# Kernel tuning notes

Measured on AMD Instinct MI355X. Metric: run time of the kernel, lower is better.

## Reference

```python
import jax, jax.numpy as jnp
import numpy as np
from jax import lax


def setup_inputs() -> dict:
    key = jax.random.key(0)
    ks = jax.random.split(key, 16)
    B, H, W, C = 4, 48, 48, 512
    N = H * W
    std = 0.02  # trunc_normal std in the torch init

    def nrm(k, shape, s=std):
        return jax.random.normal(k, shape, dtype=jnp.float32) * s

    return {
        "x": jax.random.normal(ks[0], (B, N, C), jnp.float32),
        "context": jax.random.normal(ks[1], (B, N, C), jnp.float32),
        "mask1": jax.random.uniform(ks[2], (B, N), jnp.float32),
        "mask2": jax.random.uniform(ks[3], (B, N), jnp.float32),
        "q_w": nrm(ks[4], (C, C)), "q_b": jnp.zeros((C,), jnp.float32),
        "kv1_w": nrm(ks[5], (C, C)), "kv1_b": jnp.zeros((C,), jnp.float32),
        "kv2_w": nrm(ks[6], (C, C)), "kv2_b": jnp.zeros((C,), jnp.float32),
        "f1_w": nrm(ks[7], (1, 48)), "f1_b": jnp.zeros((1,), jnp.float32),
        "f2_w": nrm(ks[8], (1, 12)), "f2_b": jnp.zeros((1,), jnp.float32),
        "lepe_w": nrm(ks[9], (C, C)), "lepe_b": jnp.zeros((C,), jnp.float32),
        "lepe_conv_w": nrm(ks[10], (C, 1, 3, 3), float(np.sqrt(2.0 / 9.0))),
        "lepe_conv_b": jnp.zeros((C,), jnp.float32),
        "proj_w": nrm(ks[11], (C, C)), "proj_b": jnp.zeros((C,), jnp.float32),
        "H": H, "W": W,
    }


def _lin(t, w, b):
    # torch nn.Linear: y = t @ W^T + b, W:[out,in]
    return t @ w.T + b


def _pooled_seq(ctx, idx, f1_w, f1_b, f2_w, f2_b):
    # ctx:[B,HW,C], idx:[B,HW] mask-sorted indices. sr_ratio==4 => groups of 48/12/1.
    B, HW, Cc = ctx.shape
    t1, t2 = HW // 192, HW // 24  # token1=(HW//48)//4, token2=(HW//12)//2
    g = jnp.take_along_axis(ctx, idx[:, :, None], axis=1)  # [B,HW,C] gathered
    p1 = g[:, : HW // 4].transpose(0, 2, 1).reshape(B, Cc, t1, 48)
    p2 = g[:, HW // 4 : 3 * HW // 4].transpose(0, 2, 1).reshape(B, Cc, t2, 12)
    p3 = g[:, 3 * HW // 4 :].transpose(0, 2, 1)  # [B,C,HW//4]
    a1 = (p1 @ f1_w.T)[..., 0] + f1_b  # [B,C,t1]
    a2 = (p2 @ f2_w.T)[..., 0] + f2_b  # [B,C,t2]
    return jnp.concatenate([a1, a2, p3], axis=-1).transpose(0, 2, 1)  # [B,Lkv,C]


def reference(x, context, mask1, mask2, q_w, q_b, kv1_w, kv1_b, kv2_w, kv2_b,
              f1_w, f1_b, f2_w, f2_b, lepe_w, lepe_b, lepe_conv_w, lepe_conv_b,
              proj_w, proj_b, H, W):
    B, N, C = x.shape
    nh = 8
    hd = C // nh
    scale = hd ** -0.5

    # lepe: linear + depthwise 3x3 conv positional encoding
    le = _lin(x, lepe_w, lepe_b).transpose(0, 2, 1).reshape(B, C, H, W)
    le = lax.conv_general_dilated(le, lepe_conv_w, (1, 1), ((1, 1), (1, 1)),
                                  dimension_numbers=("NCHW", "OIHW", "NCHW"),
                                  feature_group_count=C)
    lepe = (le + lepe_conv_b[None, :, None, None]).reshape(B, C, N).transpose(0, 2, 1)

    # mask-sorted grouped pooling of context (two orderings: row-major and transposed)
    idx1 = jnp.argsort(mask1, axis=1)
    idx2 = jnp.argsort(mask2, axis=1)
    ctx_t = context.reshape(B, H, W, C).transpose(0, 2, 1, 3).reshape(B, N, C)
    seq1 = _pooled_seq(context, idx1, f1_w, f1_b, f2_w, f2_b)
    seq2 = _pooled_seq(ctx_t, idx2, f1_w, f1_b, f2_w, f2_b)

    q = _lin(x, q_w, q_b).reshape(B, N, nh, hd).transpose(0, 2, 1, 3)  # [B,h,N,hd]
    kv1 = _lin(seq1, kv1_w, kv1_b).reshape(B, -1, 2, nh // 2, hd).transpose(2, 0, 3, 1, 4)
    kv2 = _lin(seq2, kv2_w, kv2_b).reshape(B, -1, 2, nh // 2, hd).transpose(2, 0, 3, 1, 4)
    k = jnp.concatenate([kv1[0], kv2[0]], axis=1)  # [B,h,Lkv,hd]
    v = jnp.concatenate([kv1[1], kv2[1]], axis=1)

    attn = jax.nn.softmax(jnp.einsum("bhnd,bhld->bhnl", q, k) * scale, axis=-1)
    out = jnp.einsum("bhnl,bhld->bhnd", attn, v).transpose(0, 2, 1, 3).reshape(B, N, C)
    return _lin(out + lepe, proj_w, proj_b)
```

## Files before the change

kernel.cpp:

```cpp
#include <hip/hip_runtime.h>
#include <hip/hip_bf16.h>
#include <math.h>

#define B_    4
#define H_    48
#define W_    48
#define N_    2304
#define C_    512
#define NH_   8
#define HD_   64
#define LKV_  684
#define LKP_  704

typedef __attribute__((ext_vector_type(8))) short short8;
typedef __attribute__((ext_vector_type(8))) unsigned short ushort8;
typedef __attribute__((ext_vector_type(4))) float f32x4;

#define MFMA16(a, b, c) __builtin_amdgcn_mfma_f32_16x16x32_bf16(a, b, c, 0, 0, 0)

__device__ __forceinline__ unsigned short f2bf(float f) {
  __hip_bfloat16 h = __float2bfloat16(f);
  return *reinterpret_cast<unsigned short*>(&h);
}
__device__ __forceinline__ float bf2f(unsigned short u) {
  unsigned int x = ((unsigned int)u) << 16;
  return *reinterpret_cast<float*>(&x);
}
__device__ __forceinline__ void gld16(const unsigned short* g, unsigned short* l) {
  __builtin_amdgcn_global_load_lds(
      (const __attribute__((address_space(1))) void*)g,
      (__attribute__((address_space(3))) void*)l, 16, 0, 0);
}

__global__ __launch_bounds__(256) void pack_all(
    const float* __restrict__ lepe_w, const float* __restrict__ q_w,
    const float* __restrict__ kv1_w, const float* __restrict__ kv2_w,
    const float* __restrict__ proj_w, const float* __restrict__ x,
    unsigned short* __restrict__ wb, unsigned short* __restrict__ xb)
{
  int i = (blockIdx.x * 256 + threadIdx.x) * 4;
  const float* s; unsigned short* d; int rel;
  if      (i < 262144)  { s = lepe_w; d = wb;           rel = i; }
  else if (i < 524288)  { s = q_w;    d = wb + 262144;  rel = i - 262144; }
  else if (i < 786432)  { s = kv1_w;  d = wb + 524288;  rel = i - 524288; }
  else if (i < 1048576) { s = kv2_w;  d = wb + 786432;  rel = i - 786432; }
  else if (i < 1310720) { s = proj_w; d = wb + 1048576; rel = i - 1048576; }
  else                  { s = x;      d = xb;           rel = i - 1310720; }
  float4 v = *(const float4*)(s + rel);
  ushort4 o;
  o.x = f2bf(v.x); o.y = f2bf(v.y); o.z = f2bf(v.z); o.w = f2bf(v.w);
  *(ushort4*)(d + rel) = o;
}

struct GPair {
  const unsigned short *A0, *A1, *B0, *B1;
  const float *bias0, *bias1;
  void *out0, *out1;
  int bf0, bf1;
  float sc0, sc1;
};

__global__ __launch_bounds__(256) void gemm_bf16(GPair p, int K, int Nn)
{
  const unsigned short* A  = blockIdx.z ? p.A1 : p.A0;
  const unsigned short* Bw = blockIdx.z ? p.B1 : p.B0;
  const float* bias        = blockIdx.z ? p.bias1 : p.bias0;
  void* out                = blockIdx.z ? p.out1 : p.out0;
  const int out_bf16       = blockIdx.z ? p.bf1 : p.bf0;
  const float oscale       = blockIdx.z ? p.sc1 : p.sc0;

  __shared__ unsigned short Abuf[128 * 32];
  __shared__ unsigned short Bbuf[128 * 32];
  const int tid = threadIdx.x;
  const int l = tid & 63, w = tid >> 6;
  const int wm = w >> 1, wn = w & 1;
  const int lo16 = l & 15, hi = l >> 4;
  const int row0 = blockIdx.x * 128, col0 = blockIdx.y * 128;
  const int srow = tid >> 2, scol = (tid & 3) * 8;

  const unsigned short* Asrc = A + (size_t)(row0 + srow) * K + scol;
  const unsigned short* Bsrc = Bw + (size_t)(col0 + srow) * K + scol;

  f32x4 acc[4][4];
  #pragma unroll
  for (int m = 0; m < 4; ++m)
    #pragma unroll
    for (int n = 0; n < 4; ++n)
      #pragma unroll
      for (int r = 0; r < 4; ++r) acc[m][n][r] = 0.f;

  for (int k0 = 0; k0 < K; k0 += 32) {
    __syncthreads();
    gld16(Asrc + k0,                   &Abuf[tid * 8]);
    gld16(Asrc + (size_t)64 * K + k0,  &Abuf[2048 + tid * 8]);
    gld16(Bsrc + k0,                   &Bbuf[tid * 8]);
    gld16(Bsrc + (size_t)64 * K + k0,  &Bbuf[2048 + tid * 8]);
    __syncthreads();
    short8 af[4], bf[4];
    #pragma unroll
    for (int m = 0; m < 4; ++m)
      af[m] = *(const short8*)&Abuf[(wm * 64 + m * 16 + lo16) * 32 + hi * 8];
    #pragma unroll
    for (int n = 0; n < 4; ++n)
      bf[n] = *(const short8*)&Bbuf[(wn * 64 + n * 16 + lo16) * 32 + hi * 8];
    #pragma unroll
    for (int m = 0; m < 4; ++m)
      #pragma unroll
      for (int n = 0; n < 4; ++n)
        acc[m][n] = MFMA16(af[m], bf[n], acc[m][n]);
  }

  #pragma unroll
  for (int m = 0; m < 4; ++m) {
    #pragma unroll
    for (int n = 0; n < 4; ++n) {
      int gcol = col0 + wn * 64 + n * 16 + lo16;
      #pragma unroll
      for (int r = 0; r < 4; ++r) {
        int grow = row0 + wm * 64 + m * 16 + hi * 4 + r;
        float v = acc[m][n][r] + bias[gcol];
        if (out_bf16)
          ((unsigned short*)out)[(size_t)grow * Nn + gcol] = f2bf(v * oscale);
        else
          ((float*)out)[(size_t)grow * Nn + gcol] = v;
      }
    }
  }
}

__global__ __launch_bounds__(256) void dwconv_kernel(
    const unsigned short* __restrict__ lin, const float* __restrict__ cw,
    const float* __restrict__ cb, unsigned short* __restrict__ outp)
{
  const int cg = threadIdx.x & 63;
  const int wslot = blockIdx.x * 4 + (threadIdx.x >> 6);
  const int nslots = gridDim.x * 4;

  float wf[72];
  const float* wsrc = cw + cg * 72;
  #pragma unroll
  for (int i = 0; i < 18; ++i)
    *(float4*)&wf[i * 4] = *(const float4*)(wsrc + i * 4);
  float bias[8];
  *(float4*)&bias[0] = *(const float4*)(cb + cg * 8);
  *(float4*)&bias[4] = *(const float4*)(cb + cg * 8 + 4);

  for (int pos = wslot; pos < B_ * N_; pos += nslots) {
    int wv = pos % W_;
    int r  = pos / W_;
    int hv = r % H_;
    int b  = r / H_;
    float acc[8];
    #pragma unroll
    for (int j = 0; j < 8; ++j) acc[j] = bias[j];
    #pragma unroll
    for (int dy = 0; dy < 3; ++dy) {
      int hh = hv + dy - 1;
      if (hh < 0 || hh >= H_) continue;
      #pragma unroll
      for (int dx = 0; dx < 3; ++dx) {
        int ww = wv + dx - 1;
        if (ww < 0 || ww >= W_) continue;
        ushort8 v = *(const ushort8*)(lin + ((((size_t)b * H_ + hh) * W_ + ww) * 64 + cg) * 8);
        #pragma unroll
        for (int j = 0; j < 8; ++j)
          acc[j] += wf[j * 9 + dy * 3 + dx] * bf2f(v[j]);
      }
    }
    ushort8 ov;
    #pragma unroll
    for (int j = 0; j < 8; ++j) ov[j] = f2bf(acc[j]);
    *(ushort8*)(outp + ((size_t)pos * 64 + cg) * 8) = ov;
  }
}

__global__ __launch_bounds__(256) void rank_argsort(
    const float* __restrict__ m1, const float* __restrict__ m2,
    int* __restrict__ i1, int* __restrict__ i2)
{
  __shared__ float key[N_];
  const int blk = blockIdx.x;
  const int row = blk / 36, chunk = blk % 36;
  const float* m = (row < 4) ? (m1 + (size_t)row * N_) : (m2 + (size_t)(row - 4) * N_);
  int* out = (row < 4) ? (i1 + (size_t)row * N_) : (i2 + (size_t)(row - 4) * N_);
  for (int i = threadIdx.x; i < N_ / 4; i += 256)
    ((float4*)key)[i] = ((const float4*)m)[i];
  __syncthreads();
  const int e = chunk * 64 + (threadIdx.x >> 2);
  const int sl = threadIdx.x & 3;
  const float ki = key[e];
  int rank = 0;
  #pragma unroll 4
  for (int t = 0; t < N_ / 16; ++t) {
    int jb = sl * 4 + t * 16;
    float4 kv = *(const float4*)&key[jb];
    rank += (kv.x < ki) || (kv.x == ki && jb     < e);
    rank += (kv.y < ki) || (kv.y == ki && jb + 1 < e);
    rank += (kv.z < ki) || (kv.z == ki && jb + 2 < e);
    rank += (kv.w < ki) || (kv.w == ki && jb + 3 < e);
  }
  rank += __shfl_xor(rank, 1);
  rank += __shfl_xor(rank, 2);
  if (sl == 0) out[rank] = e;
}

__global__ __launch_bounds__(256) void pool_kernel(
    const float* __restrict__ ctx,
    const int* __restrict__ idx1, const int* __restrict__ idx2,
    const float* __restrict__ f1w, const float* __restrict__ f1b,
    const float* __restrict__ f2w, const float* __restrict__ f2b_,
    unsigned short* __restrict__ seqb1, unsigned short* __restrict__ seqb2)
{
  int bl = blockIdx.x;
  const int transposed = bl >= B_ * LKP_;
  if (transposed) bl -= B_ * LKP_;
  const int* idx = transposed ? idx2 : idx1;
  unsigned short* seqb = transposed ? seqb2 : seqb1;
  int b = bl / LKP_, l = bl % LKP_;
  unsigned short* dst = seqb + ((size_t)b * LKP_ + l) * C_;
  int c0 = threadIdx.x, c1 = threadIdx.x + 256;
  if (l >= LKV_) { dst[c0] = 0; dst[c1] = 0; return; }
  const int* id = idx + (size_t)b * N_;
  int j0, cnt;
  const float* fw; float fb;
  if (l < 12)       { j0 = l * 48;              cnt = 48; fw = f1w; fb = f1b[0]; }
  else if (l < 108) { j0 = 576 + (l - 12) * 12; cnt = 12; fw = f2w; fb = f2b_[0]; }
  else              { j0 = 1728 + (l - 108);    cnt = 1;  fw = nullptr; fb = 0.f; }
  const float* cb = ctx + (size_t)b * N_ * C_;
  float a0 = fb, a1 = fb;
  int r = 0;
  for (; r + 4 <= cnt; r += 4) {
    int4 nv = *(const int4*)(id + j0 + r);
    int n0 = nv.x, n1 = nv.y, n2 = nv.z, n3 = nv.w;
    if (transposed) {
      n0 = (n0 % 48) * 48 + n0 / 48; n1 = (n1 % 48) * 48 + n1 / 48;
      n2 = (n2 % 48) * 48 + n2 / 48; n3 = (n3 % 48) * 48 + n3 / 48;
    }
    const float* s0 = cb + (size_t)n0 * C_;
    const float* s1 = cb + (size_t)n1 * C_;
    const float* s2 = cb + (size_t)n2 * C_;
    const float* s3 = cb + (size_t)n3 * C_;
    float w0 = fw[r], w1 = fw[r+1], w2 = fw[r+2], w3 = fw[r+3];
    a0 += w0 * s0[c0] + w1 * s1[c0] + w2 * s2[c0] + w3 * s3[c0];
    a1 += w0 * s0[c1] + w1 * s1[c1] + w2 * s2[c1] + w3 * s3[c1];
  }
  for (; r < cnt; ++r) {
    int n = id[j0 + r];
    if (transposed) n = (n % 48) * 48 + n / 48;
    const float* src = cb + (size_t)n * C_;
    float wr = fw ? fw[r] : 1.f;
    a0 += wr * src[c0];
    a1 += wr * src[c1];
  }
  dst[c0] = f2bf(a0);
  dst[c1] = f2bf(a1);
}

__global__ __launch_bounds__(256) void kvpack(
    const unsigned short* __restrict__ kv1, const unsigned short* __restrict__ kv2,
    unsigned short* __restrict__ Kf, unsigned short* __restrict__ Vf)
{
  __shared__ unsigned short Vt[64][72];
  const int bh = blockIdx.x / 11, t = blockIdx.x % 11;
  const int h = bh & 7, b = bh >> 3;
  const unsigned short* src = (h < 4) ? kv1 : kv2;
  const int hcol = (h & 3) * 64;
  const int tid = threadIdx.x;

  #pragma unroll
  for (int pass = 0; pass < 2; ++pass) {
    int r = pass * 32 + (tid >> 3);
    int cc = (tid & 7) * 8;
    int l = t * 64 + r;
    uint4 v = make_uint4(0, 0, 0, 0);
    if (l < LKV_)
      v = *(const uint4*)&src[(size_t)(b * LKP_ + l) * C_ + 256 + hcol + cc];
    *(uint4*)&Vt[r][cc] = v;
  }
  __syncthreads();

  #pragma unroll
  for (int pass = 0; pass < 2; ++pass) {
    int o = pass * 256 + tid;
    int lane = o & 63, ns = o >> 6;
    int frag = ns >> 1, s = ns & 1;
    int lo16 = lane & 15, hi8 = (lane >> 4) * 8;
    size_t oidx = ((size_t)blockIdx.x * 8 + ns) * 512 + lane * 8;
    {
      int l = t * 64 + frag * 16 + lo16;
      uint4 val = make_uint4(0, 0, 0, 0);
      if (l < LKV_)
        val = *(const uint4*)&src[(size_t)(b * LKP_ + l) * C_ + hcol + s * 32 + hi8];
      *(uint4*)&Kf[oidx] = val;
    }
    {
      unsigned short tmp[8];
      #pragma unroll
      for (int j = 0; j < 8; ++j)
        tmp[j] = Vt[s * 32 + hi8 + j][frag * 16 + lo16];
      *(uint4*)&Vf[oidx] = *(uint4*)tmp;
    }
  }
}

__global__ __launch_bounds__(64) void attn_kernel(
    const unsigned short* __restrict__ Qb, const unsigned short* __restrict__ Kf,
    const unsigned short* __restrict__ Vf, const unsigned short* __restrict__ lepe,
    unsigned short* __restrict__ outb)
{
  __shared__ unsigned short P[16][72];
  const int l = threadIdx.x;
  const int lo16 = l & 15, hi = l >> 4;
  const int blk = blockIdx.x;
  const int qt = blk % (N_ / 16);
  const int bh = blk / (N_ / 16);
  const int h = bh & 7, b = bh >> 3;

  const unsigned short* qptr = Qb + ((size_t)b * N_ + qt * 16 + lo16) * C_ + h * 64;
  short8 qf0 = *(const short8*)(qptr + hi * 8);
  short8 qf1 = *(const short8*)(qptr + 32 + hi * 8);

  const unsigned short* kbase = Kf + (size_t)bh * 11 * 4096 + (size_t)l * 8;
  const unsigned short* vbase = Vf + (size_t)bh * 11 * 4096 + (size_t)l * 8;

  float mreg = -INFINITY, lsum = 0.f;
  f32x4 o[4];
  #pragma unroll
  for (int df = 0; df < 4; ++df)
    #pragma unroll
    for (int r = 0; r < 4; ++r) o[df][r] = 0.f;

  for (int t = 0; t < 11; ++t) {
    short8 vf0[4], vf1[4], ka0[4], ka1[4];
    #pragma unroll
    for (int i = 0; i < 4; ++i) {
      ka0[i] = *(const short8*)(kbase + (size_t)(t * 8 + i * 2 + 0) * 512);
      ka1[i] = *(const short8*)(kbase + (size_t)(t * 8 + i * 2 + 1) * 512);
      vf0[i] = *(const short8*)(vbase + (size_t)(t * 8 + i * 2 + 0) * 512);
      vf1[i] = *(const short8*)(vbase + (size_t)(t * 8 + i * 2 + 1) * 512);
    }
    const f32x4 z = {0.f, 0.f, 0.f, 0.f};
    f32x4 s[4];
    #pragma unroll
    for (int n = 0; n < 4; ++n) {
      s[n] = MFMA16(ka0[n], qf0, z);
      s[n] = MFMA16(ka1[n], qf1, s[n]);
    }
    if (t == 10) {
      #pragma unroll
      for (int n = 0; n < 4; ++n)
        #pragma unroll
        for (int r = 0; r < 4; ++r)
          if (n * 16 + hi * 4 + r >= LKV_ - 640) s[n][r] = -1e30f;
    }
    float mx = -1e30f;
    #pragma unroll
    for (int n = 0; n < 4; ++n)
      #pragma unroll
      for (int r = 0; r < 4; ++r) mx = fmaxf(mx, s[n][r]);
    mx = fmaxf(mx, __shfl_xor(mx, 16));
    mx = fmaxf(mx, __shfl_xor(mx, 32));
    float mn = fmaxf(mreg, mx);
    float al = exp2f(mreg - mn);
    mreg = mn;
    float psl = 0.f;
    #pragma unroll
    for (int n = 0; n < 4; ++n) {
      #pragma unroll
      for (int rp = 0; rp < 2; ++rp) {
        float e0 = exp2f(s[n][2 * rp]     - mn);
        float e1 = exp2f(s[n][2 * rp + 1] - mn);
        psl += e0 + e1;
        unsigned int pk = (unsigned int)f2bf(e0) | ((unsigned int)f2bf(e1) << 16);
        *(unsigned int*)&P[lo16][n * 16 + hi * 4 + 2 * rp] = pk;
      }
    }
    lsum = lsum * al + psl;
    float alb0 = __shfl(al, hi * 4 + 0);
    float alb1 = __shfl(al, hi * 4 + 1);
    float alb2 = __shfl(al, hi * 4 + 2);
    float alb3 = __shfl(al, hi * 4 + 3);
    #pragma unroll
    for (int df = 0; df < 4; ++df) {
      o[df][0] *= alb0; o[df][1] *= alb1; o[df][2] *= alb2; o[df][3] *= alb3;
    }
    short8 pa0 = *(const short8*)&P[lo16][hi * 8];
    short8 pa1 = *(const short8*)&P[lo16][32 + hi * 8];
    #pragma unroll
    for (int df = 0; df < 4; ++df) {
      o[df] = MFMA16(pa0, vf0[df], o[df]);
      o[df] = MFMA16(pa1, vf1[df], o[df]);
    }
  }

  lsum += __shfl_xor(lsum, 16);
  lsum += __shfl_xor(lsum, 32);
  float rr[4];
  #pragma unroll
  for (int r = 0; r < 4; ++r) rr[r] = 1.f / __shfl(lsum, hi * 4 + r);
  #pragma unroll
  for (int df = 0; df < 4; ++df)
    #pragma unroll
    for (int r = 0; r < 4; ++r) {
      size_t off = ((size_t)b * N_ + qt * 16 + hi * 4 + r) * C_ + h * 64 + df * 16 + lo16;
      outb[off] = f2bf(o[df][r] * rr[r] + bf2f(lepe[off]));
    }
}

extern "C" void kernel_launch(void* const* d_in, const int* in_sizes, int n_in,
                              void* d_out, int out_size, void* d_ws, size_t ws_size,
                              hipStream_t stream)
{
  const float* x      = (const float*)d_in[0];
  const float* ctx    = (const float*)d_in[1];
  const float* mask1  = (const float*)d_in[2];
  const float* mask2  = (const float*)d_in[3];
  const float* q_w    = (const float*)d_in[4];
  const float* q_b    = (const float*)d_in[5];
  const float* kv1_w  = (const float*)d_in[6];
  const float* kv1_b  = (const float*)d_in[7];
  const float* kv2_w  = (const float*)d_in[8];
  const float* kv2_b  = (const float*)d_in[9];
  const float* f1_w   = (const float*)d_in[10];
  const float* f1_b   = (const float*)d_in[11];
  const float* f2_w   = (const float*)d_in[12];
  const float* f2_b   = (const float*)d_in[13];
  const float* lepe_w = (const float*)d_in[14];
  const float* lepe_b = (const float*)d_in[15];
  const float* lcw    = (const float*)d_in[16];
  const float* lcb    = (const float*)d_in[17];
  const float* proj_w = (const float*)d_in[18];
  const float* proj_b = (const float*)d_in[19];
  float* outp = (float*)d_out;

  char* ws = (char*)d_ws;
  unsigned short* bufA  = (unsigned short*)(ws);
  unsigned short* bufB  = (unsigned short*)(ws + 18874368);
  unsigned short* xb    = (unsigned short*)(ws + 37748736);
  unsigned short* Qb    = (unsigned short*)(ws + 47185920);
  unsigned short* wb    = (unsigned short*)(ws + 56623104);
  unsigned short* seqb1 = (unsigned short*)(ws + 59244544);
  unsigned short* seqb2 = (unsigned short*)(ws + 62128128);
  unsigned short* kv1b  = (unsigned short*)(ws + 65011712);
  unsigned short* kv2b  = (unsigned short*)(ws + 67895296);
  unsigned short* Kf    = (unsigned short*)(ws + 70778880);
  unsigned short* Vf    = (unsigned short*)(ws + 73662464);
  int*            idx1  = (int*)(ws + 76546048);
  int*            idx2  = (int*)(ws + 76582912);

  unsigned short* wb_lepe = wb;
  unsigned short* wb_q    = wb + 262144;
  unsigned short* wb_kv1  = wb + 524288;
  unsigned short* wb_kv2  = wb + 786432;
  unsigned short* wb_proj = wb + 1048576;

  dim3 blk(256);
  const int XN = B_ * N_ * C_;
  const int PACKQ = (1310720 + XN) / 4 / 256;

  pack_all<<<dim3(PACKQ), blk, 0, stream>>>(lepe_w, q_w, kv1_w, kv2_w, proj_w, x, wb, xb);
  rank_argsort<<<dim3(288), blk, 0, stream>>>(mask1, mask2, idx1, idx2);

  pool_kernel<<<dim3(2 * B_ * LKP_), blk, 0, stream>>>(
      ctx, idx1, idx2, f1_w, f1_b, f2_w, f2_b, seqb1, seqb2);

  {
    GPair p = { seqb1, seqb2, wb_kv1, wb_kv2, kv1_b, kv2_b,
                (void*)kv1b, (void*)kv2b, 1, 1, 1.f, 1.f };
    gemm_bf16<<<dim3(22, 4, 2), blk, 0, stream>>>(p, C_, C_);
  }
  kvpack<<<dim3(32 * 11), blk, 0, stream>>>(kv1b, kv2b, Kf, Vf);

  {
    GPair p = { xb, xb, wb_lepe, wb_q, lepe_b, q_b,
                (void*)bufA, (void*)Qb, 1, 1, 1.f, 0.18033688011112042f };
    gemm_bf16<<<dim3(72, 4, 2), blk, 0, stream>>>(p, C_, C_);
  }
  dwconv_kernel<<<dim3(384), blk, 0, stream>>>(bufA, lcw, lcb, bufB);

  attn_kernel<<<dim3(B_ * NH_ * (N_ / 16)), dim3(64), 0, stream>>>(Qb, Kf, Vf, bufB, xb);

  {
    GPair p = { xb, xb, wb_proj, wb_proj, proj_b, proj_b,
                (void*)outp, (void*)outp, 0, 0, 1.f, 1.f };
    gemm_bf16<<<dim3(72, 4, 1), blk, 0, stream>>>(p, C_, C_);
  }
}
```

Baseline: 180.3 us.

## Fuse pack and argsort kernels; prefetch K and use 4-wave attention blocks

Merges the bf16 pack kernel and the rank-based argsort into a single launch to save one kernel launch. The attention kernel moves from one wave per block to four waves per block, each handling 16 query rows of a 64-row tile. It also software-prefetches the next K tile into registers while the current tile is processed. The online-softmax rescale of the output accumulator is skipped when no lane's running max increases. In exchange, register pressure rises from the extra prefetch buffers and the per-tile wave-level branch adds some divergence risk.

```diff
diff --git a/kernel.cpp b/kernel.cpp
--- a/kernel.cpp
+++ b/kernel.cpp
@@ -32,154 +32,33 @@
       (__attribute__((address_space(3))) void*)l, 16, 0, 0);
 }
 
-__global__ __launch_bounds__(256) void pack_all(
+#define PACKQ 5888
+
+__global__ __launch_bounds__(256) void pack_sort(
     const float* __restrict__ lepe_w, const float* __restrict__ q_w,
     const float* __restrict__ kv1_w, const float* __restrict__ kv2_w,
     const float* __restrict__ proj_w, const float* __restrict__ x,
-    unsigned short* __restrict__ wb, unsigned short* __restrict__ xb)
-{
-  int i = (blockIdx.x * 256 + threadIdx.x) * 4;
-  const float* s; unsigned short* d; int rel;
-  if      (i < 262144)  { s = lepe_w; d = wb;           rel = i; }
-  else if (i < 524288)  { s = q_w;    d = wb + 262144;  rel = i - 262144; }
-  else if (i < 786432)  { s = kv1_w;  d = wb + 524288;  rel = i - 524288; }
-  else if (i < 1048576) { s = kv2_w;  d = wb + 786432;  rel = i - 786432; }
-  else if (i < 1310720) { s = proj_w; d = wb + 1048576; rel = i - 1048576; }
-  else                  { s = x;      d = xb;           rel = i - 1310720; }
-  float4 v = *(const float4*)(s + rel);
-  ushort4 o;
-  o.x = f2bf(v.x); o.y = f2bf(v.y); o.z = f2bf(v.z); o.w = f2bf(v.w);
-  *(ushort4*)(d + rel) = o;
-}
-
-struct GPair {
-  const unsigned short *A0, *A1, *B0, *B1;
-  const float *bias0, *bias1;
-  void *out0, *out1;
-  int bf0, bf1;
-  float sc0, sc1;
-};
-
-__global__ __launch_bounds__(256) void gemm_bf16(GPair p, int K, int Nn)
-{
-  const unsigned short* A  = blockIdx.z ? p.A1 : p.A0;
-  const unsigned short* Bw = blockIdx.z ? p.B1 : p.B0;
-  const float* bias        = blockIdx.z ? p.bias1 : p.bias0;
-  void* out                = blockIdx.z ? p.out1 : p.out0;
-  const int out_bf16       = blockIdx.z ? p.bf1 : p.bf0;
-  const float oscale       = blockIdx.z ? p.sc1 : p.sc0;
-
-  __shared__ unsigned short Abuf[128 * 32];
-  __shared__ unsigned short Bbuf[128 * 32];
-  const int tid = threadIdx.x;
-  const int l = tid & 63, w = tid >> 6;
-  const int wm = w >> 1, wn = w & 1;
-  const int lo16 = l & 15, hi = l >> 4;
-  const int row0 = blockIdx.x * 128, col0 = blockIdx.y * 128;
-  const int srow = tid >> 2, scol = (tid & 3) * 8;
-
-  const unsigned short* Asrc = A + (size_t)(row0 + srow) * K + scol;
-  const unsigned short* Bsrc = Bw + (size_t)(col0 + srow) * K + scol;
-
-  f32x4 acc[4][4];
-  #pragma unroll
-  for (int m = 0; m < 4; ++m)
-    #pragma unroll
-    for (int n = 0; n < 4; ++n)
-      #pragma unroll
-      for (int r = 0; r < 4; ++r) acc[m][n][r] = 0.f;
-
-  for (int k0 = 0; k0 < K; k0 += 32) {
-    __syncthreads();
-    gld16(Asrc + k0,                   &Abuf[tid * 8]);
-    gld16(Asrc + (size_t)64 * K + k0,  &Abuf[2048 + tid * 8]);
-    gld16(Bsrc + k0,                   &Bbuf[tid * 8]);
-    gld16(Bsrc + (size_t)64 * K + k0,  &Bbuf[2048 + tid * 8]);
-    __syncthreads();
-    short8 af[4], bf[4];
-    #pragma unroll
-    for (int m = 0; m < 4; ++m)
-      af[m] = *(const short8*)&Abuf[(wm * 64 + m * 16 + lo16) * 32 + hi * 8];
-    #pragma unroll
-    for (int n = 0; n < 4; ++n)
-      bf[n] = *(const short8*)&Bbuf[(wn * 64 + n * 16 + lo16) * 32 + hi * 8];
-    #pragma unroll
-    for (int m = 0; m < 4; ++m)
-      #pragma unroll
-      for (int n = 0; n < 4; ++n)
-        acc[m][n] = MFMA16(af[m], bf[n], acc[m][n]);
-  }
-
-  #pragma unroll
-  for (int m = 0; m < 4; ++m) {
-    #pragma unroll
-    for (int n = 0; n < 4; ++n) {
-      int gcol = col0 + wn * 64 + n * 16 + lo16;
-      #pragma unroll
-      for (int r = 0; r < 4; ++r) {
-        int grow = row0 + wm * 64 + m * 16 + hi * 4 + r;
-        float v = acc[m][n][r] + bias[gcol];
-        if (out_bf16)
-          ((unsigned short*)out)[(size_t)grow * Nn + gcol] = f2bf(v * oscale);
-        else
-          ((float*)out)[(size_t)grow * Nn + gcol] = v;
-      }
-    }
-  }
-}
-
-__global__ __launch_bounds__(256) void dwconv_kernel(
-    const unsigned short* __restrict__ lin, const float* __restrict__ cw,
-    const float* __restrict__ cb, unsigned short* __restrict__ outp)
-{
-  const int cg = threadIdx.x & 63;
-  const int wslot = blockIdx.x * 4 + (threadIdx.x >> 6);
-  const int nslots = gridDim.x * 4;
-
-  float wf[72];
-  const float* wsrc = cw + cg * 72;
-  #pragma unroll
-  for (int i = 0; i < 18; ++i)
-    *(float4*)&wf[i * 4] = *(const float4*)(wsrc + i * 4);
-  float bias[8];
-  *(float4*)&bias[0] = *(const float4*)(cb + cg * 8);
-  *(float4*)&bias[4] = *(const float4*)(cb + cg * 8 + 4);
-
-  for (int pos = wslot; pos < B_ * N_; pos += nslots) {
-    int wv = pos % W_;
-    int r  = pos / W_;
-    int hv = r % H_;
-    int b  = r / H_;
-    float acc[8];
-    #pragma unroll
-    for (int j = 0; j < 8; ++j) acc[j] = bias[j];
-    #pragma unroll
-    for (int dy = 0; dy < 3; ++dy) {
-      int hh = hv + dy - 1;
-      if (hh < 0 || hh >= H_) continue;
-      #pragma unroll
-      for (int dx = 0; dx < 3; ++dx) {
-        int ww = wv + dx - 1;
-        if (ww < 0 || ww >= W_) continue;
-        ushort8 v = *(const ushort8*)(lin + ((((size_t)b * H_ + hh) * W_ + ww) * 64 + cg) * 8);
-        #pragma unroll
-        for (int j = 0; j < 8; ++j)
-          acc[j] += wf[j * 9 + dy * 3 + dx] * bf2f(v[j]);
-      }
-    }
-    ushort8 ov;
-    #pragma unroll
-    for (int j = 0; j < 8; ++j) ov[j] = f2bf(acc[j]);
-    *(ushort8*)(outp + ((size_t)pos * 64 + cg) * 8) = ov;
-  }
-}
-
-__global__ __launch_bounds__(256) void rank_argsort(
+    unsigned short* __restrict__ wb, unsigned short* __restrict__ xb,
     const float* __restrict__ m1, const float* __restrict__ m2,
     int* __restrict__ i1, int* __restrict__ i2)
 {
   __shared__ float key[N_];
-  const int blk = blockIdx.x;
+  if (blockIdx.x < PACKQ) {
+    int i = (blockIdx.x * 256 + threadIdx.x) * 4;
+    const float* s; unsigned short* d; int rel;
+    if      (i < 262144)  { s = lepe_w; d = wb;           rel = i; }
+    else if (i < 524288)  { s = q_w;    d = wb + 262144;  rel = i - 262144; }
+    else if (i < 786432)  { s = kv1_w;  d = wb + 524288;  rel = i - 524288; }
+    else if (i < 1048576) { s = kv2_w;  d = wb + 786432;  rel = i - 786432; }
+    else if (i < 1310720) { s = proj_w; d = wb + 1048576; rel = i - 1048576; }
+    else                  { s = x;      d = xb;           rel = i - 1310720; }
+    float4 v = *(const float4*)(s + rel);
+    ushort4 o;
+    o.x = f2bf(v.x); o.y = f2bf(v.y); o.z = f2bf(v.z); o.w = f2bf(v.w);
+    *(ushort4*)(d + rel) = o;
+    return;
+  }
+  const int blk = blockIdx.x - PACKQ;
   const int row = blk / 36, chunk = blk % 36;
   const float* m = (row < 4) ? (m1 + (size_t)row * N_) : (m2 + (size_t)(row - 4) * N_);
   int* out = (row < 4) ? (i1 + (size_t)row * N_) : (i2 + (size_t)(row - 4) * N_);
@@ -202,6 +81,128 @@
   rank += __shfl_xor(rank, 1);
   rank += __shfl_xor(rank, 2);
   if (sl == 0) out[rank] = e;
+}
+
+struct GPair {
+  const unsigned short *A0, *A1, *B0, *B1;
+  const float *bias0, *bias1;
+  void *out0, *out1;
+  int bf0, bf1;
+  float sc0, sc1;
+};
+
+__global__ __launch_bounds__(256) void gemm_bf16(GPair p, int K, int Nn)
+{
+  const unsigned short* A  = blockIdx.z ? p.A1 : p.A0;
+  const unsigned short* Bw = blockIdx.z ? p.B1 : p.B0;
+  const float* bias        = blockIdx.z ? p.bias1 : p.bias0;
+  void* out                = blockIdx.z ? p.out1 : p.out0;
+  const int out_bf16       = blockIdx.z ? p.bf1 : p.bf0;
+  const float oscale       = blockIdx.z ? p.sc1 : p.sc0;
+
+  __shared__ unsigned short Abuf[128 * 32];
+  __shared__ unsigned short Bbuf[128 * 32];
+  const int tid = threadIdx.x;
+  const int l = tid & 63, w = tid >> 6;
+  const int wm = w >> 1, wn = w & 1;
+  const int lo16 = l & 15, hi = l >> 4;
+  const int row0 = blockIdx.x * 128, col0 = blockIdx.y * 128;
+  const int srow = tid >> 2, scol = (tid & 3) * 8;
+
+  const unsigned short* Asrc = A + (size_t)(row0 + srow) * K + scol;
+  const unsigned short* Bsrc = Bw + (size_t)(col0 + srow) * K + scol;
+
+  f32x4 acc[4][4];
+  #pragma unroll
+  for (int m = 0; m < 4; ++m)
+    #pragma unroll
+    for (int n = 0; n < 4; ++n)
+      #pragma unroll
+      for (int r = 0; r < 4; ++r) acc[m][n][r] = 0.f;
+
+  for (int k0 = 0; k0 < K; k0 += 32) {
+    __syncthreads();
+    gld16(Asrc + k0,                   &Abuf[tid * 8]);
+    gld16(Asrc + (size_t)64 * K + k0,  &Abuf[2048 + tid * 8]);
+    gld16(Bsrc + k0,                   &Bbuf[tid * 8]);
+    gld16(Bsrc + (size_t)64 * K + k0,  &Bbuf[2048 + tid * 8]);
+    __syncthreads();
+    short8 af[4], bf[4];
+    #pragma unroll
+    for (int m = 0; m < 4; ++m)
+      af[m] = *(const short8*)&Abuf[(wm * 64 + m * 16 + lo16) * 32 + hi * 8];
+    #pragma unroll
+    for (int n = 0; n < 4; ++n)
+      bf[n] = *(const short8*)&Bbuf[(wn * 64 + n * 16 + lo16) * 32 + hi * 8];
+    #pragma unroll
+    for (int m = 0; m < 4; ++m)
+      #pragma unroll
+      for (int n = 0; n < 4; ++n)
+        acc[m][n] = MFMA16(af[m], bf[n], acc[m][n]);
+  }
+
+  #pragma unroll
+  for (int m = 0; m < 4; ++m) {
+    #pragma unroll
+    for (int n = 0; n < 4; ++n) {
+      int gcol = col0 + wn * 64 + n * 16 + lo16;
+      #pragma unroll
+      for (int r = 0; r < 4; ++r) {
+        int grow = row0 + wm * 64 + m * 16 + hi * 4 + r;
+        float v = acc[m][n][r] + bias[gcol];
+        if (out_bf16)
+          ((unsigned short*)out)[(size_t)grow * Nn + gcol] = f2bf(v * oscale);
+        else
+          ((float*)out)[(size_t)grow * Nn + gcol] = v;
+      }
+    }
+  }
+}
+
+__global__ __launch_bounds__(256) void dwconv_kernel(
+    const unsigned short* __restrict__ lin, const float* __restrict__ cw,
+    const float* __restrict__ cb, unsigned short* __restrict__ outp)
+{
+  const int cg = threadIdx.x & 63;
+  const int wslot = blockIdx.x * 4 + (threadIdx.x >> 6);
+  const int nslots = gridDim.x * 4;
+
+  float wf[72];
+  const float* wsrc = cw + cg * 72;
+  #pragma unroll
+  for (int i = 0; i < 18; ++i)
+    *(float4*)&wf[i * 4] = *(const float4*)(wsrc + i * 4);
+  float bias[8];
+  *(float4*)&bias[0] = *(const float4*)(cb + cg * 8);
+  *(float4*)&bias[4] = *(const float4*)(cb + cg * 8 + 4);
+
+  for (int pos = wslot; pos < B_ * N_; pos += nslots) {
+    int wv = pos % W_;
+    int r  = pos / W_;
+    int hv = r % H_;
+    int b  = r / H_;
+    float acc[8];
+    #pragma unroll
+    for (int j = 0; j < 8; ++j) acc[j] = bias[j];
+    #pragma unroll
+    for (int dy = 0; dy < 3; ++dy) {
+      int hh = hv + dy - 1;
+      if (hh < 0 || hh >= H_) continue;
+      #pragma unroll
+      for (int dx = 0; dx < 3; ++dx) {
+        int ww = wv + dx - 1;
+        if (ww < 0 || ww >= W_) continue;
+        ushort8 v = *(const ushort8*)(lin + ((((size_t)b * H_ + hh) * W_ + ww) * 64 + cg) * 8);
+        #pragma unroll
+        for (int j = 0; j < 8; ++j)
+          acc[j] += wf[j * 9 + dy * 3 + dx] * bf2f(v[j]);
+      }
+    }
+    ushort8 ov;
+    #pragma unroll
+    for (int j = 0; j < 8; ++j) ov[j] = f2bf(acc[j]);
+    *(ushort8*)(outp + ((size_t)pos * 64 + cg) * 8) = ov;
+  }
 }
 
 __global__ __launch_bounds__(256) void pool_kernel(
@@ -303,20 +304,21 @@
   }
 }
 
-__global__ __launch_bounds__(64) void attn_kernel(
+__global__ __launch_bounds__(256) void attn_kernel(
     const unsigned short* __restrict__ Qb, const unsigned short* __restrict__ Kf,
     const unsigned short* __restrict__ Vf, const unsigned short* __restrict__ lepe,
     unsigned short* __restrict__ outb)
 {
-  __shared__ unsigned short P[16][72];
-  const int l = threadIdx.x;
+  __shared__ unsigned short P[4][16][72];
+  const int tid = threadIdx.x;
+  const int l = tid & 63, wv = tid >> 6;
   const int lo16 = l & 15, hi = l >> 4;
-  const int blk = blockIdx.x;
-  const int qt = blk % (N_ / 16);
-  const int bh = blk / (N_ / 16);
+  const int qt64 = blockIdx.x % (N_ / 64);
+  const int bh = blockIdx.x / (N_ / 64);
   const int h = bh & 7, b = bh >> 3;
-
-  const unsigned short* qptr = Qb + ((size_t)b * N_ + qt * 16 + lo16) * C_ + h * 64;
+  const int qrow0 = qt64 * 64 + wv * 16;
+
+  const unsigned short* qptr = Qb + ((size_t)b * N_ + qrow0 + lo16) * C_ + h * 64;
   short8 qf0 = *(const short8*)(qptr + hi * 8);
   short8 qf1 = *(const short8*)(qptr + 32 + hi * 8);
 
@@ -330,14 +332,26 @@
     #pragma unroll
     for (int r = 0; r < 4; ++r) o[df][r] = 0.f;
 
+  short8 ka0[4], ka1[4], kn0[4], kn1[4];
+  #pragma unroll
+  for (int n = 0; n < 4; ++n) {
+    ka0[n] = *(const short8*)(kbase + (size_t)(n * 2 + 0) * 512);
+    ka1[n] = *(const short8*)(kbase + (size_t)(n * 2 + 1) * 512);
+  }
+
   for (int t = 0; t < 11; ++t) {
-    short8 vf0[4], vf1[4], ka0[4], ka1[4];
+    short8 vf0[4], vf1[4];
     #pragma unroll
     for (int i = 0; i < 4; ++i) {
-      ka0[i] = *(const short8*)(kbase + (size_t)(t * 8 + i * 2 + 0) * 512);
-      ka1[i] = *(const short8*)(kbase + (size_t)(t * 8 + i * 2 + 1) * 512);
       vf0[i] = *(const short8*)(vbase + (size_t)(t * 8 + i * 2 + 0) * 512);
       vf1[i] = *(const short8*)(vbase + (size_t)(t * 8 + i * 2 + 1) * 512);
+    }
+    if (t < 10) {
+      #pragma unroll
+      for (int n = 0; n < 4; ++n) {
+        kn0[n] = *(const short8*)(kbase + (size_t)((t + 1) * 8 + n * 2 + 0) * 512);
+        kn1[n] = *(const short8*)(kbase + (size_t)((t + 1) * 8 + n * 2 + 1) * 512);
+      }
     }
     const f32x4 z = {0.f, 0.f, 0.f, 0.f};
     f32x4 s[4];
@@ -360,37 +374,40 @@
       for (int r = 0; r < 4; ++r) mx = fmaxf(mx, s[n][r]);
     mx = fmaxf(mx, __shfl_xor(mx, 16));
     mx = fmaxf(mx, __shfl_xor(mx, 32));
-    float mn = fmaxf(mreg, mx);
-    float al = exp2f(mreg - mn);
-    mreg = mn;
+    if (__any(mx > mreg)) {
+      float mn = fmaxf(mreg, mx);
+      float al = exp2f(mreg - mn);
+      mreg = mn;
+      lsum *= al;
+      float a0 = __shfl(al, hi * 4 + 0), a1 = __shfl(al, hi * 4 + 1);
+      float a2 = __shfl(al, hi * 4 + 2), a3 = __shfl(al, hi * 4 + 3);
+      #pragma unroll
+      for (int df = 0; df < 4; ++df) {
+        o[df][0] *= a0; o[df][1] *= a1; o[df][2] *= a2; o[df][3] *= a3;
+      }
+    }
     float psl = 0.f;
     #pragma unroll
     for (int n = 0; n < 4; ++n) {
       #pragma unroll
       for (int rp = 0; rp < 2; ++rp) {
-        float e0 = exp2f(s[n][2 * rp]     - mn);
-        float e1 = exp2f(s[n][2 * rp + 1] - mn);
+        float e0 = exp2f(s[n][2 * rp]     - mreg);
+        float e1 = exp2f(s[n][2 * rp + 1] - mreg);
         psl += e0 + e1;
-        unsigned int pk = (unsigned int)f2bf(e0) | ((unsigned int)f2bf(e1) << 16);
-        *(unsigned int*)&P[lo16][n * 16 + hi * 4 + 2 * rp] = pk;
+        *(unsigned int*)&P[wv][lo16][n * 16 + hi * 4 + 2 * rp] =
+            (unsigned int)f2bf(e0) | ((unsigned int)f2bf(e1) << 16);
       }
     }
-    lsum = lsum * al + psl;
-    float alb0 = __shfl(al, hi * 4 + 0);
-    float alb1 = __shfl(al, hi * 4 + 1);
-    float alb2 = __shfl(al, hi * 4 + 2);
-    float alb3 = __shfl(al, hi * 4 + 3);
-    #pragma unroll
-    for (int df = 0; df < 4; ++df) {
-      o[df][0] *= alb0; o[df][1] *= alb1; o[df][2] *= alb2; o[df][3] *= alb3;
-    }
-    short8 pa0 = *(const short8*)&P[lo16][hi * 8];
-    short8 pa1 = *(const short8*)&P[lo16][32 + hi * 8];
+    lsum += psl;
+    short8 pa0 = *(const short8*)&P[wv][lo16][hi * 8];
+    short8 pa1 = *(const short8*)&P[wv][lo16][32 + hi * 8];
     #pragma unroll
     for (int df = 0; df < 4; ++df) {
       o[df] = MFMA16(pa0, vf0[df], o[df]);
       o[df] = MFMA16(pa1, vf1[df], o[df]);
     }
+    #pragma unroll
+    for (int n = 0; n < 4; ++n) { ka0[n] = kn0[n]; ka1[n] = kn1[n]; }
   }
 
   lsum += __shfl_xor(lsum, 16);
@@ -402,7 +419,7 @@
   for (int df = 0; df < 4; ++df)
     #pragma unroll
     for (int r = 0; r < 4; ++r) {
-      size_t off = ((size_t)b * N_ + qt * 16 + hi * 4 + r) * C_ + h * 64 + df * 16 + lo16;
+      size_t off = ((size_t)b * N_ + qrow0 + hi * 4 + r) * C_ + h * 64 + df * 16 + lo16;
       outb[off] = f2bf(o[df][r] * rr[r] + bf2f(lepe[off]));
     }
 }
@@ -455,11 +472,9 @@
   unsigned short* wb_proj = wb + 1048576;
 
   dim3 blk(256);
-  const int XN = B_ * N_ * C_;
-  const int PACKQ = (1310720 + XN) / 4 / 256;
-
-  pack_all<<<dim3(PACKQ), blk, 0, stream>>>(lepe_w, q_w, kv1_w, kv2_w, proj_w, x, wb, xb);
-  rank_argsort<<<dim3(288), blk, 0, stream>>>(mask1, mask2, idx1, idx2);
+
+  pack_sort<<<dim3(PACKQ + 288), blk, 0, stream>>>(
+      lepe_w, q_w, kv1_w, kv2_w, proj_w, x, wb, xb, mask1, mask2, idx1, idx2);
 
   pool_kernel<<<dim3(2 * B_ * LKP_), blk, 0, stream>>>(
       ctx, idx1, idx2, f1_w, f1_b, f2_w, f2_b, seqb1, seqb2);
@@ -478,7 +493,7 @@
   }
   dwconv_kernel<<<dim3(384), blk, 0, stream>>>(bufA, lcw, lcb, bufB);
 
-  attn_kernel<<<dim3(B_ * NH_ * (N_ / 16)), dim3(64), 0, stream>>>(Qb, Kf, Vf, bufB, xb);
+  attn_kernel<<<dim3(B_ * NH_ * (N_ / 64)), blk, 0, stream>>>(Qb, Kf, Vf, bufB, xb);
 
   {
     GPair p = { xb, xb, wb_proj, wb_proj, proj_b, proj_b,
```

After: 190.6 us. 5.7% more time.
